# Kernel optimization log

Hardware: AMD Instinct MI355X
Metric: run time of the kernel (lower is better)

## Reference

```python
import jax, jax.numpy as jnp
import numpy as np

NUM_HEADS = 12
HEAD_DIM = 64
EPS = 1e-6


def _layernorm(x, g, b):
    mu = jnp.mean(x, axis=-1, keepdims=True)
    var = jnp.mean(jnp.square(x - mu), axis=-1, keepdims=True)
    return (x - mu) * jax.lax.rsqrt(var + EPS) * g + b


def setup_inputs() -> dict:
    key = jax.random.key(0)
    ks = jax.random.split(key, 8)
    D, DFF = 768, 3072
    s = lambda d: 1.0 / np.sqrt(d)
    return {
        "hidden_states": jax.random.normal(ks[0], (4, 2048, D), jnp.float32),
        "ln1_g": jnp.ones((D,), jnp.float32),
        "ln1_b": jnp.zeros((D,), jnp.float32),
        "w_qkv": jax.random.normal(ks[1], (D, 3 * D), jnp.float32) * s(D),
        "b_qkv": jnp.zeros((3 * D,), jnp.float32),
        "w_attn": jax.random.normal(ks[2], (D, D), jnp.float32) * s(D),
        "b_attn": jnp.zeros((D,), jnp.float32),
        "ln2_g": jnp.ones((D,), jnp.float32),
        "ln2_b": jnp.zeros((D,), jnp.float32),
        "w_in": jax.random.normal(ks[3], (D, DFF), jnp.float32) * s(D),
        "b_in": jnp.zeros((DFF,), jnp.float32),
        "w_out": jax.random.normal(ks[4], (DFF, D), jnp.float32) * s(DFF),
        "b_out": jnp.zeros((D,), jnp.float32),
    }


def reference(hidden_states, ln1_g, ln1_b, w_qkv, b_qkv, w_attn, b_attn,
              ln2_g, ln2_b, w_in, b_in, w_out, b_out):
    B, S, D = hidden_states.shape
    residual = hidden_states
    h = _layernorm(hidden_states, ln1_g, ln1_b)
    # QKV: [B,S,3D] -> [B,S,3,H,hd] -> [3,B,H,S,hd]
    qkv = (h @ w_qkv + b_qkv).reshape(B, S, 3, NUM_HEADS, HEAD_DIM)
    qkv = jnp.transpose(qkv, (2, 0, 3, 1, 4))
    scale = HEAD_DIM ** (-0.5)
    q, k, v = qkv[0] * scale, qkv[1], qkv[2]
    scores = jnp.einsum("bhqd,bhkd->bhqk", q, k)
    attn = jax.nn.softmax(scores, axis=-1)
    o = jnp.einsum("bhqk,bhkd->bhqd", attn, v)
    o = jnp.transpose(o, (0, 2, 1, 3)).reshape(B, S, D)
    h = residual + (o @ w_attn + b_attn)
    residual2 = h
    h2 = _layernorm(h, ln2_g, ln2_b)
    h2 = jax.nn.gelu(h2 @ w_in + b_in, approximate=False)
    h2 = h2 @ w_out + b_out
    return residual2 + h2
```

## Files before the change

kernel.cpp:

```cpp
#include <hip/hip_runtime.h>

typedef __bf16 bf16_t;
typedef bf16_t bf16x8 __attribute__((ext_vector_type(8)));
typedef float f32x4 __attribute__((ext_vector_type(4)));
typedef unsigned short ushortx8 __attribute__((ext_vector_type(8)));
typedef unsigned short ushortx4 __attribute__((ext_vector_type(4)));
typedef short short4v __attribute__((ext_vector_type(4)));

union UB8 { bf16_t h8[8]; bf16x8 b; };

__device__ __forceinline__ unsigned short f2bf(float f) {
  union { bf16_t h; unsigned short u; } cv;
  cv.h = (bf16_t)f;
  return cv.u;
}

__device__ __forceinline__ void gl_lds16(const unsigned short* g, unsigned short* l) {
  __builtin_amdgcn_global_load_lds((const __attribute__((address_space(1))) void*)g,
                                   (__attribute__((address_space(3))) void*)l,
                                   16, 0, 0);
}

__device__ __forceinline__ float gelu_fast(float v) {
  float v3 = v * v * v;
  float z = -2.30211886f * v - 0.102945f * v3;
  float e = exp2f(z);
  return v * __builtin_amdgcn_rcpf(1.0f + e);
}

__global__ __launch_bounds__(256) void ln_kernel(const float* __restrict__ x,
                                                 const float* __restrict__ g,
                                                 const float* __restrict__ b,
                                                 unsigned short* __restrict__ out) {
  int row = blockIdx.x;
  int t = threadIdx.x;
  const float* xr = x + (size_t)row * 768;
  float v0 = xr[t], v1 = xr[t + 256], v2 = xr[t + 512];
  __shared__ float red[4];
  float s = v0 + v1 + v2;
  for (int o = 32; o > 0; o >>= 1) s += __shfl_down(s, o, 64);
  if ((t & 63) == 0) red[t >> 6] = s;
  __syncthreads();
  float mu = (red[0] + red[1] + red[2] + red[3]) * (1.0f / 768.0f);
  __syncthreads();
  float d0 = v0 - mu, d1 = v1 - mu, d2 = v2 - mu;
  s = d0 * d0 + d1 * d1 + d2 * d2;
  for (int o = 32; o > 0; o >>= 1) s += __shfl_down(s, o, 64);
  if ((t & 63) == 0) red[t >> 6] = s;
  __syncthreads();
  float var = (red[0] + red[1] + red[2] + red[3]) * (1.0f / 768.0f);
  float rs = rsqrtf(var + 1e-6f);
  unsigned short* orow = out + (size_t)row * 768;
  orow[t]       = f2bf(d0 * rs * g[t]       + b[t]);
  orow[t + 256] = f2bf(d1 * rs * g[t + 256] + b[t + 256]);
  orow[t + 512] = f2bf(d2 * rs * g[t + 512] + b[t + 512]);
}

__global__ __launch_bounds__(256) void transpose_all(
    const float* __restrict__ w_qkv, const float* __restrict__ w_attn,
    const float* __restrict__ w_in, const float* __restrict__ w_out,
    unsigned short* __restrict__ wqkvT, unsigned short* __restrict__ wattnT,
    unsigned short* __restrict__ winT, unsigned short* __restrict__ woutT) {
  int id = blockIdx.x;
  const float* W; unsigned short* WT; int K, N, nx, ny;
  if (id < 1728)      { W = w_qkv;  WT = wqkvT;  K = 768;  N = 2304; nx = id % 72; ny = id / 72; }
  else if (id < 2304) { id -= 1728; W = w_attn; WT = wattnT; K = 768;  N = 768;  nx = id % 24; ny = id / 24; }
  else if (id < 4608) { id -= 2304; W = w_in;   WT = winT;   K = 768;  N = 3072; nx = id % 96; ny = id / 96; }
  else                { id -= 4608; W = w_out;  WT = woutT;  K = 3072; N = 768;  nx = id % 24; ny = id / 24; }
  __shared__ float tile[32][33];
  int n0 = nx * 32, k0 = ny * 32;
  int tx = threadIdx.x, ty = threadIdx.y;
  for (int i = 0; i < 4; i++)
    tile[ty + i * 8][tx] = W[(size_t)(k0 + ty + i * 8) * N + n0 + tx];
  __syncthreads();
  for (int i = 0; i < 4; i++)
    WT[(size_t)(n0 + ty + i * 8) * K + k0 + tx] = f2bf(tile[tx][ty + i * 8]);
}

template <int EPI, int TM>
__device__ __forceinline__ void gemm_body(const unsigned short* __restrict__ A,
                                          const unsigned short* __restrict__ BT,
                                          const float* __restrict__ bias,
                                          const float* resid,
                                          void* out, unsigned short* vt, int os,
                                          int N, int K) {
  constexpr int BK = 32, MI = TM / 32;
  constexpr int ASZ = TM * BK;
  constexpr int BUF = ASZ + 128 * BK;
  __shared__ __align__(16) unsigned short smem[4 * BUF];

  int t = threadIdx.x;
  int w = t >> 6, lane = t & 63, ln = lane & 15, quad = lane >> 4;
  int wm = w & 1, wn = w >> 1;

  int gx = gridDim.x;
  int nwg = gx * gridDim.y;
  int flat = blockIdx.y * gx + blockIdx.x;
  int nf = (flat & 7) * (nwg >> 3) + (flat >> 3);
  int m0 = (nf / gx) * TM, n0 = (nf % gx) * 128;

  int lrow = lane >> 2;
  int lslot = lane & 3;
  int scol = (lslot ^ ((lrow >> 1) & 3)) * 8;

  const unsigned short* gA0 = A + (size_t)(m0 + w * 16 + lrow) * K + scol;
  const unsigned short* gA1 = gA0 + (size_t)64 * K;
  const unsigned short* gB0 = BT + (size_t)(n0 + w * 16 + lrow) * K + scol;
  const unsigned short* gB1 = gB0 + (size_t)64 * K;

  auto stage = [&](int buf) {
    unsigned short* Sb = smem + buf * BUF;
    gl_lds16(gA0, Sb + w * 512);
    gA0 += BK;
    if constexpr (TM == 128) { gl_lds16(gA1, Sb + 2048 + w * 512); gA1 += BK; }
    gl_lds16(gB0, Sb + ASZ + w * 512);
    gl_lds16(gB1, Sb + ASZ + 2048 + w * 512);
    gB0 += BK; gB1 += BK;
  };

  f32x4 acc[MI][4];
  f32x4 zero = {0.f, 0.f, 0.f, 0.f};
  for (int mi = 0; mi < MI; mi++)
    for (int ni = 0; ni < 4; ni++) acc[mi][ni] = zero;

  int soff = (quad ^ ((ln >> 1) & 3)) * 8;

  auto compute = [&](int kt) {
    const unsigned short* Sc = smem + (kt & 3) * BUF;
    bf16x8 af[MI], bfr[4];
#pragma unroll
    for (int mi = 0; mi < MI; mi++)
      af[mi] = *(const bf16x8*)&Sc[(wm * (TM / 2) + mi * 16 + ln) * 32 + soff];
#pragma unroll
    for (int ni = 0; ni < 4; ni++)
      bfr[ni] = *(const bf16x8*)&Sc[ASZ + (wn * 64 + ni * 16 + ln) * 32 + soff];
    __builtin_amdgcn_s_setprio(1);
#pragma unroll
    for (int mi = 0; mi < MI; mi++)
#pragma unroll
      for (int ni = 0; ni < 4; ni++)
        acc[mi][ni] = __builtin_amdgcn_mfma_f32_16x16x32_bf16(af[mi], bfr[ni],
                                                              acc[mi][ni], 0, 0, 0);
    __builtin_amdgcn_s_setprio(0);
  };

  int nk = K / BK;
  stage(0); stage(1);
  for (int kt = 0; kt < nk; kt += 2) {
    asm volatile("s_waitcnt vmcnt(0)" ::: "memory");
    __builtin_amdgcn_s_barrier();
    __builtin_amdgcn_sched_barrier(0);
    if (kt + 2 < nk) {
      stage((kt + 2) & 3);
      stage((kt + 3) & 3);
    }
    compute(kt);
    compute(kt + 1);
  }

  if (EPI == 2) {
    float* outp = (float*)out;
    for (int mi = 0; mi < MI; mi++) {
      for (int ni = 0; ni < 4; ni++) {
        int col = n0 + wn * 64 + ni * 16 + ln;
        float bv = bias[col];
        for (int r = 0; r < 4; r++) {
          int row = m0 + wm * (TM / 2) + mi * 16 + quad * 4 + r;
          float v = acc[mi][ni][r] + bv;
          v += resid[(size_t)row * N + col];
          outp[(size_t)row * N + col] = v;
        }
      }
    }
  } else {
    __syncthreads();
    unsigned short* Cs16 = smem + w * 1024;
    unsigned short* outp = (unsigned short*)out;
    for (int mi = 0; mi < MI; mi++) {
      for (int ni = 0; ni < 4; ni++) {
        int col = n0 + wn * 64 + ni * 16 + ln;
        float bv = bias[col];
        for (int r = 0; r < 4; r++) {
          float v = acc[mi][ni][r] + bv;
          if (EPI == 0) {
            if (col < 768) v *= 0.18033688f;
          } else {
            v = gelu_fast(v);
          }
          Cs16[(quad * 4 + r) * 64 + ni * 16 + ln] = f2bf(v);
        }
      }
      __syncthreads();
      if (EPI == 0 && n0 >= 1536) {
        int c = n0 - 1536 + wn * 64 + lane;
        int s0 = m0 + wm * (TM / 2) + mi * 16;
        int bb = s0 >> 11, sl = s0 & 2047;
        ushortx8 lo, hi;
        for (int r = 0; r < 8; r++) lo[r] = Cs16[r * 64 + lane];
        for (int r = 0; r < 8; r++) hi[r] = Cs16[(8 + r) * 64 + lane];
        size_t vbase = ((size_t)(bb * 768 + c)) * 2048 + sl;
        *(ushortx8*)&vt[vbase] = lo;
        *(ushortx8*)&vt[vbase + 8] = hi;
      } else {
        int OS = (EPI == 0) ? os : N;
        for (int j = 0; j < 2; j++) {
          int rrow = j * 8 + (lane >> 3);
          int ch = (lane & 7) * 8;
          ushortx8 pv = *(const ushortx8*)&Cs16[rrow * 64 + ch];
          *(ushortx8*)&outp[(size_t)(m0 + wm * (TM / 2) + mi * 16 + rrow) * OS +
                            n0 + wn * 64 + ch] = pv;
        }
      }
      __syncthreads();
    }
  }
}

__global__ __launch_bounds__(256) void gemm_qkv(const unsigned short* A,
    const unsigned short* BT, const float* bias, void* out, unsigned short* vt,
    int N, int K) {
  gemm_body<0, 128>(A, BT, bias, nullptr, out, vt, 1536, N, K);
}
__global__ __launch_bounds__(256) void gemm_attnout(const unsigned short* A,
    const unsigned short* BT, const float* bias, const float* resid, void* out,
    int N, int K) {
  gemm_body<2, 64>(A, BT, bias, resid, out, nullptr, N, N, K);
}
__global__ __launch_bounds__(256) void gemm_ffn1(const unsigned short* A,
    const unsigned short* BT, const float* bias, void* out, int N, int K) {
  gemm_body<1, 128>(A, BT, bias, nullptr, out, nullptr, N, N, K);
}
__global__ __launch_bounds__(256) void gemm_ffn2(const unsigned short* A,
    const unsigned short* BT, const float* bias, const float* resid, void* out,
    int N, int K) {
  gemm_body<2, 128>(A, BT, bias, resid, out, nullptr, N, N, K);
}

__global__ __launch_bounds__(512, 4) void flash_attn(
    const unsigned short* __restrict__ qk, const unsigned short* __restrict__ v_t,
    unsigned short* __restrict__ o) {
  int flat = blockIdx.y * 16 + blockIdx.x;
  int nf = (flat & 7) * 96 + (flat >> 3);
  int qt = nf % 16;
  int bh = nf / 16;
  int b = bh / 12, h = bh % 12;
  int t = threadIdx.x;
  int w = t >> 6, lane = t & 63, ln = lane & 15, quad = lane >> 4;
  int qg = w & 3, kh2 = w >> 2;

  __shared__ __align__(16) unsigned short smem[18432];
  int qrow0 = b * 2048 + qt * 128;
  int qw = qrow0 + qg * 32;

  bf16x8 qf[2][2];
  for (int qi = 0; qi < 2; qi++)
    for (int kh = 0; kh < 2; kh++)
      qf[qi][kh] = *(const bf16x8*)&qk[(size_t)(qw + qi * 16 + ln) * 1536 +
                                      h * 64 + kh * 32 + quad * 8];

  UB8 ones8;
#pragma unroll
  for (int r = 0; r < 8; r++) ones8.h8[r] = (bf16_t)1.0f;

  f32x4 zero = {0.f, 0.f, 0.f, 0.f};
  f32x4 o_acc[4][2];
  for (int df = 0; df < 4; df++)
    for (int qi = 0; qi < 2; qi++) o_acc[df][qi] = zero;
  f32x4 l_acc[2] = {zero, zero};

  int sr = t >> 3, sc = (t & 7) * 8;
  int ssr = (sr & 32) | (((sr >> 2) & 1) << 4) | (((sr >> 3) & 3) << 2) | (sr & 3);
  ushortx8 kreg = *(const ushortx8*)&qk[(size_t)(b * 2048 + sr) * 1536 + 768 + h * 64 + sc];
  ushortx8 vreg = *(const ushortx8*)&v_t[(size_t)(bh * 64 + sr) * 2048 + sc];

  for (int kt = 0; kt < 32; kt++) {
    unsigned short* Ks = smem + (kt & 1) * 9216;
    unsigned short* Vt = Ks + 4608;
    *(ushortx8*)&Ks[ssr * 72 + sc] = kreg;
    *(ushortx8*)&Vt[sr * 72 + sc] = vreg;
    __syncthreads();
    if (kt < 31) {
      int krow0 = b * 2048 + (kt + 1) * 64;
      kreg = *(const ushortx8*)&qk[(size_t)(krow0 + sr) * 1536 + 768 + h * 64 + sc];
      vreg = *(const ushortx8*)&v_t[(size_t)(bh * 64 + sr) * 2048 + (kt + 1) * 64 + sc];
    }

    UB8 pb[2];
#pragma unroll
    for (int kf = 0; kf < 2; kf++) {
      int krow = kh2 * 32 + kf * 16;
      f32x4 ST[2] = {zero, zero};
      bf16x8 kA0 = *(const bf16x8*)&Ks[(krow + ln) * 72 + quad * 8];
      bf16x8 kA1 = *(const bf16x8*)&Ks[(krow + ln) * 72 + 32 + quad * 8];
      __builtin_amdgcn_s_setprio(1);
#pragma unroll
      for (int qi = 0; qi < 2; qi++) {
        ST[qi] = __builtin_amdgcn_mfma_f32_16x16x32_bf16(kA0, qf[qi][0], ST[qi], 0, 0, 0);
        ST[qi] = __builtin_amdgcn_mfma_f32_16x16x32_bf16(kA1, qf[qi][1], ST[qi], 0, 0, 0);
      }
      __builtin_amdgcn_s_setprio(0);
#pragma unroll
      for (int qi = 0; qi < 2; qi++)
#pragma unroll
        for (int r = 0; r < 4; r++)
          pb[qi].h8[kf * 4 + r] = (bf16_t)__builtin_amdgcn_exp2f(ST[qi][r]);
    }
    __builtin_amdgcn_s_setprio(1);
#pragma unroll
    for (int qi = 0; qi < 2; qi++)
      l_acc[qi] = __builtin_amdgcn_mfma_f32_16x16x32_bf16(ones8.b, pb[qi].b,
                                                          l_acc[qi], 0, 0, 0);
#pragma unroll
    for (int df = 0; df < 4; df++) {
      bf16x8 vA = *(const bf16x8*)&Vt[(df * 16 + ln) * 72 + kh2 * 32 + quad * 8];
#pragma unroll
      for (int qi = 0; qi < 2; qi++)
        o_acc[df][qi] = __builtin_amdgcn_mfma_f32_16x16x32_bf16(vA, pb[qi].b,
                                                                o_acc[df][qi], 0, 0, 0);
    }
    __builtin_amdgcn_s_setprio(0);
  }

  __syncthreads();
  float* fb = (float*)smem;
  float* fbl = fb + 8320;
  if (kh2 == 1) {
    for (int df = 0; df < 4; df++)
      for (int qi = 0; qi < 2; qi++)
        for (int r = 0; r < 4; r++)
          fb[qg * 2080 + (qi * 16 + ln) * 65 + df * 16 + quad * 4 + r] =
              o_acc[df][qi][r];
    if (quad == 0)
      for (int qi = 0; qi < 2; qi++)
        fbl[qg * 32 + qi * 16 + ln] = l_acc[qi][0];
  }
  __syncthreads();
  float inv[2];
  if (kh2 == 0) {
    for (int qi = 0; qi < 2; qi++) {
      float lt = l_acc[qi][0] + fbl[qg * 32 + qi * 16 + ln];
      inv[qi] = __builtin_amdgcn_rcpf(lt);
    }
    for (int df = 0; df < 4; df++)
      for (int qi = 0; qi < 2; qi++)
        for (int r = 0; r < 4; r++)
          o_acc[df][qi][r] += fb[qg * 2080 + (qi * 16 + ln) * 65 + df * 16 + quad * 4 + r];
  }
  __syncthreads();
  if (kh2 == 0) {
    unsigned short* Osm = smem + qg * 2304;
    for (int qi = 0; qi < 2; qi++)
      for (int df = 0; df < 4; df++)
        for (int r = 0; r < 4; r++)
          Osm[(qi * 16 + ln) * 72 + df * 16 + quad * 4 + r] =
              f2bf(o_acc[df][qi][r] * inv[qi]);
  }
  __syncthreads();
  if (kh2 == 0) {
    unsigned short* Osm = smem + qg * 2304;
    for (int p2 = 0; p2 < 4; p2++) {
      int rr = p2 * 8 + (lane >> 3);
      int ch = (lane & 7) * 8;
      ushortx8 u = *(const ushortx8*)&Osm[rr * 72 + ch];
      *(ushortx8*)&o[(size_t)(qw + rr) * 768 + h * 64 + ch] = u;
    }
  }
}

extern "C" void kernel_launch(void* const* d_in, const int* in_sizes, int n_in,
                              void* d_out, int out_size, void* d_ws, size_t ws_size,
                              hipStream_t stream) {
  const float* hidden = (const float*)d_in[0];
  const float* ln1_g  = (const float*)d_in[1];
  const float* ln1_b  = (const float*)d_in[2];
  const float* w_qkv  = (const float*)d_in[3];
  const float* b_qkv  = (const float*)d_in[4];
  const float* w_attn = (const float*)d_in[5];
  const float* b_attn = (const float*)d_in[6];
  const float* ln2_g  = (const float*)d_in[7];
  const float* ln2_b  = (const float*)d_in[8];
  const float* w_in   = (const float*)d_in[9];
  const float* b_in   = (const float*)d_in[10];
  const float* w_out  = (const float*)d_in[11];
  const float* b_out  = (const float*)d_in[12];
  float* out = (float*)d_out;

  char* ws = (char*)d_ws;
  unsigned short* wqkvT  = (unsigned short*)(ws + 0);
  unsigned short* wattnT = (unsigned short*)(ws + 3538944);
  unsigned short* winT   = (unsigned short*)(ws + 4718592);
  unsigned short* woutT  = (unsigned short*)(ws + 9437184);
  unsigned short* bufX   = (unsigned short*)(ws + 14155776);
  unsigned short* bufBig = (unsigned short*)(ws + 26738688);
  unsigned short* bufQK  = bufBig;
  unsigned short* v_t    = (unsigned short*)(ws + 26738688 + 25165824);

  transpose_all<<<6912, dim3(32, 8), 0, stream>>>(w_qkv, w_attn, w_in, w_out,
                                                  wqkvT, wattnT, winT, woutT);
  ln_kernel<<<8192, 256, 0, stream>>>(hidden, ln1_g, ln1_b, bufX);
  gemm_qkv<<<dim3(18, 64), 256, 0, stream>>>(bufX, wqkvT, b_qkv, (void*)bufQK,
                                             v_t, 2304, 768);
  flash_attn<<<dim3(16, 48), 512, 0, stream>>>(bufQK, v_t, bufX);
  gemm_attnout<<<dim3(6, 128), 256, 0, stream>>>(bufX, wattnT, b_attn, hidden,
                                                 (void*)out, 768, 768);
  ln_kernel<<<8192, 256, 0, stream>>>(out, ln2_g, ln2_b, bufX);
  gemm_ffn1<<<dim3(24, 64), 256, 0, stream>>>(bufX, winT, b_in, (void*)bufBig,
                                              3072, 768);
  gemm_ffn2<<<dim3(6, 64), 256, 0, stream>>>(bufBig, woutT, b_out, out,
                                             (void*)out, 768, 3072);
}
```

Measured before the change: 373.9 us.

## Load FFN2 B-operand fragments directly into registers, bypassing LDS

For the FFN2 GEMM (K=3072), the B tiles are now loaded straight from global memory into registers in MFMA fragment layout. A three-deep rotation of register buffers with vmcnt(6) waits replaces the four-stage LDS ring; only A still goes through LDS. This cuts LDS footprint and LDS read traffic and may allow higher occupancy. The cost is more VGPRs and global loads that are less coalesced, since each lane reads 16 bytes from a different row. It assumes K/32 is a multiple of 3, which holds for K=3072.

```diff
diff --git a/kernel.cpp b/kernel.cpp
--- a/kernel.cpp
+++ b/kernel.cpp
@@ -77,7 +77,7 @@
     WT[(size_t)(n0 + ty + i * 8) * K + k0 + tx] = f2bf(tile[tx][ty + i * 8]);
 }
 
-template <int EPI, int TM>
+template <int EPI, int TM, bool BREG>
 __device__ __forceinline__ void gemm_body(const unsigned short* __restrict__ A,
                                           const unsigned short* __restrict__ BT,
                                           const float* __restrict__ bias,
@@ -87,7 +87,8 @@
   constexpr int BK = 32, MI = TM / 32;
   constexpr int ASZ = TM * BK;
   constexpr int BUF = ASZ + 128 * BK;
-  __shared__ __align__(16) unsigned short smem[4 * BUF];
+  constexpr int SMSZ = BREG ? (3 * ASZ) : (4 * BUF);
+  __shared__ __align__(16) unsigned short smem[SMSZ];
 
   int t = threadIdx.x;
   int w = t >> 6, lane = t & 63, ln = lane & 15, quad = lane >> 4;
@@ -105,18 +106,6 @@
 
   const unsigned short* gA0 = A + (size_t)(m0 + w * 16 + lrow) * K + scol;
   const unsigned short* gA1 = gA0 + (size_t)64 * K;
-  const unsigned short* gB0 = BT + (size_t)(n0 + w * 16 + lrow) * K + scol;
-  const unsigned short* gB1 = gB0 + (size_t)64 * K;
-
-  auto stage = [&](int buf) {
-    unsigned short* Sb = smem + buf * BUF;
-    gl_lds16(gA0, Sb + w * 512);
-    gA0 += BK;
-    if constexpr (TM == 128) { gl_lds16(gA1, Sb + 2048 + w * 512); gA1 += BK; }
-    gl_lds16(gB0, Sb + ASZ + w * 512);
-    gl_lds16(gB1, Sb + ASZ + 2048 + w * 512);
-    gB0 += BK; gB1 += BK;
-  };
 
   f32x4 acc[MI][4];
   f32x4 zero = {0.f, 0.f, 0.f, 0.f};
@@ -124,38 +113,103 @@
     for (int ni = 0; ni < 4; ni++) acc[mi][ni] = zero;
 
   int soff = (quad ^ ((ln >> 1) & 3)) * 8;
-
-  auto compute = [&](int kt) {
-    const unsigned short* Sc = smem + (kt & 3) * BUF;
-    bf16x8 af[MI], bfr[4];
-#pragma unroll
-    for (int mi = 0; mi < MI; mi++)
-      af[mi] = *(const bf16x8*)&Sc[(wm * (TM / 2) + mi * 16 + ln) * 32 + soff];
+  int nk = K / BK;
+
+  if constexpr (BREG) {
+    const unsigned short* gB[4];
 #pragma unroll
     for (int ni = 0; ni < 4; ni++)
-      bfr[ni] = *(const bf16x8*)&Sc[ASZ + (wn * 64 + ni * 16 + ln) * 32 + soff];
-    __builtin_amdgcn_s_setprio(1);
-#pragma unroll
-    for (int mi = 0; mi < MI; mi++)
+      gB[ni] = BT + (size_t)(n0 + wn * 64 + ni * 16 + ln) * K + quad * 8;
+
+    bf16x8 breg[3][4];
+    auto stageA = [&](int buf) {
+      unsigned short* Sb = smem + buf * ASZ;
+      gl_lds16(gA0, Sb + w * 512);
+      gl_lds16(gA1, Sb + 2048 + w * 512);
+      gA0 += BK; gA1 += BK;
+    };
+    auto loadB = [&](int set) {
+#pragma unroll
+      for (int ni = 0; ni < 4; ni++) {
+        breg[set][ni] = *(const bf16x8*)gB[ni];
+        gB[ni] += BK;
+      }
+    };
+    auto bstep = [&](int u, int l, bool cnt6, bool doPre) {
+      if (cnt6) asm volatile("s_waitcnt vmcnt(6)" ::: "memory");
+      else      asm volatile("s_waitcnt vmcnt(0)" ::: "memory");
+      __builtin_amdgcn_s_barrier();
+      __builtin_amdgcn_sched_barrier(0);
+      if (doPre) { stageA(l); loadB(l); }
+      const unsigned short* Sc = smem + u * ASZ;
+      bf16x8 af[MI];
+#pragma unroll
+      for (int mi = 0; mi < MI; mi++)
+        af[mi] = *(const bf16x8*)&Sc[(wm * 64 + mi * 16 + ln) * 32 + soff];
+      __builtin_amdgcn_s_setprio(1);
+#pragma unroll
+      for (int mi = 0; mi < MI; mi++) {
+        acc[mi][0] = __builtin_amdgcn_mfma_f32_16x16x32_bf16(af[mi], breg[u][0], acc[mi][0], 0, 0, 0);
+        acc[mi][1] = __builtin_amdgcn_mfma_f32_16x16x32_bf16(af[mi], breg[u][1], acc[mi][1], 0, 0, 0);
+        acc[mi][2] = __builtin_amdgcn_mfma_f32_16x16x32_bf16(af[mi], breg[u][2], acc[mi][2], 0, 0, 0);
+        acc[mi][3] = __builtin_amdgcn_mfma_f32_16x16x32_bf16(af[mi], breg[u][3], acc[mi][3], 0, 0, 0);
+      }
+      __builtin_amdgcn_s_setprio(0);
+    };
+
+    stageA(0); loadB(0);
+    stageA(1); loadB(1);
+    for (int g = 0; g < nk / 3 - 1; ++g) {
+      bstep(0, 2, true, true);
+      bstep(1, 0, true, true);
+      bstep(2, 1, true, true);
+    }
+    bstep(0, 2, true, true);
+    bstep(1, 0, true, false);
+    bstep(2, 1, false, false);
+  } else {
+    const unsigned short* gB0 = BT + (size_t)(n0 + w * 16 + lrow) * K + scol;
+    const unsigned short* gB1 = gB0 + (size_t)64 * K;
+    auto stage = [&](int buf) {
+      unsigned short* Sb = smem + buf * BUF;
+      gl_lds16(gA0, Sb + w * 512);
+      gA0 += BK;
+      if constexpr (TM == 128) { gl_lds16(gA1, Sb + 2048 + w * 512); gA1 += BK; }
+      gl_lds16(gB0, Sb + ASZ + w * 512);
+      gl_lds16(gB1, Sb + ASZ + 2048 + w * 512);
+      gB0 += BK; gB1 += BK;
+    };
+    auto compute = [&](int kt) {
+      const unsigned short* Sc = smem + (kt & 3) * BUF;
+      bf16x8 af[MI], bfr[4];
+#pragma unroll
+      for (int mi = 0; mi < MI; mi++)
+        af[mi] = *(const bf16x8*)&Sc[(wm * (TM / 2) + mi * 16 + ln) * 32 + soff];
 #pragma unroll
       for (int ni = 0; ni < 4; ni++)
-        acc[mi][ni] = __builtin_amdgcn_mfma_f32_16x16x32_bf16(af[mi], bfr[ni],
-                                                              acc[mi][ni], 0, 0, 0);
-    __builtin_amdgcn_s_setprio(0);
-  };
-
-  int nk = K / BK;
-  stage(0); stage(1);
-  for (int kt = 0; kt < nk; kt += 2) {
-    asm volatile("s_waitcnt vmcnt(0)" ::: "memory");
-    __builtin_amdgcn_s_barrier();
-    __builtin_amdgcn_sched_barrier(0);
-    if (kt + 2 < nk) {
-      stage((kt + 2) & 3);
-      stage((kt + 3) & 3);
-    }
-    compute(kt);
-    compute(kt + 1);
+        bfr[ni] = *(const bf16x8*)&Sc[ASZ + (wn * 64 + ni * 16 + ln) * 32 + soff];
+      __builtin_amdgcn_s_setprio(1);
+#pragma unroll
+      for (int mi = 0; mi < MI; mi++)
+#pragma unroll
+        for (int ni = 0; ni < 4; ni++)
+          acc[mi][ni] = __builtin_amdgcn_mfma_f32_16x16x32_bf16(af[mi], bfr[ni],
+                                                                acc[mi][ni], 0, 0, 0);
+      __builtin_amdgcn_s_setprio(0);
+    };
+
+    stage(0); stage(1);
+    for (int kt = 0; kt < nk; kt += 2) {
+      asm volatile("s_waitcnt vmcnt(0)" ::: "memory");
+      __builtin_amdgcn_s_barrier();
+      __builtin_amdgcn_sched_barrier(0);
+      if (kt + 2 < nk) {
+        stage((kt + 2) & 3);
+        stage((kt + 3) & 3);
+      }
+      compute(kt);
+      compute(kt + 1);
+    }
   }
 
   if (EPI == 2) {
@@ -219,21 +273,21 @@
 __global__ __launch_bounds__(256) void gemm_qkv(const unsigned short* A,
     const unsigned short* BT, const float* bias, void* out, unsigned short* vt,
     int N, int K) {
-  gemm_body<0, 128>(A, BT, bias, nullptr, out, vt, 1536, N, K);
+  gemm_body<0, 128, false>(A, BT, bias, nullptr, out, vt, 1536, N, K);
 }
 __global__ __launch_bounds__(256) void gemm_attnout(const unsigned short* A,
     const unsigned short* BT, const float* bias, const float* resid, void* out,
     int N, int K) {
-  gemm_body<2, 64>(A, BT, bias, resid, out, nullptr, N, N, K);
+  gemm_body<2, 64, false>(A, BT, bias, resid, out, nullptr, N, N, K);
 }
 __global__ __launch_bounds__(256) void gemm_ffn1(const unsigned short* A,
     const unsigned short* BT, const float* bias, void* out, int N, int K) {
-  gemm_body<1, 128>(A, BT, bias, nullptr, out, nullptr, N, N, K);
+  gemm_body<1, 128, false>(A, BT, bias, nullptr, out, nullptr, N, N, K);
 }
 __global__ __launch_bounds__(256) void gemm_ffn2(const unsigned short* A,
     const unsigned short* BT, const float* bias, const float* resid, void* out,
     int N, int K) {
-  gemm_body<2, 128>(A, BT, bias, resid, out, nullptr, N, N, K);
+  gemm_body<2, 128, true>(A, BT, bias, resid, out, nullptr, N, N, K);
 }
 
 __global__ __launch_bounds__(512, 4) void flash_attn(
```

After: 422.8 us. 1.13x slower.
